# Performance work log

Measured on AMD Instinct MI355X. Metric: run time of the kernel, lower is better.

Reference implementation:

```python
import jax, jax.numpy as jnp
import numpy as np

# dims: StyleGAN2 modulated conv at 64x64, 512 channels
B, IC, OC, K, SD, H, W = 16, 512, 512, 3, 512, 64, 64
EPS = 1e-8


def setup_inputs() -> dict:
    key = jax.random.key(0)
    k1, k2, k3, k4 = jax.random.split(key, 4)
    return {
        "input": jax.random.normal(k1, (B, IC, H, W), dtype=jnp.float32),
        "style": jax.random.normal(k2, (B, SD), dtype=jnp.float32),
        # learned params
        "weight": jax.random.normal(k3, (1, OC, IC, K, K), dtype=jnp.float32),
        "mod_weight": jax.random.normal(k4, (IC, SD), dtype=jnp.float32),
        "mod_bias": jnp.ones((IC,), dtype=jnp.float32),  # bias_init=1
    }


def reference(input, style, weight, mod_weight, mod_bias):
    conv_scale = 1.0 / np.sqrt(IC * K * K)   # 1/sqrt(fan_in)
    mod_scale = 1.0 / np.sqrt(SD)            # EqualLinear scale, lr_mul=1

    # style modulation: EqualLinear(style_dim -> in_channel), no activation
    s = style @ (mod_weight * mod_scale).T + mod_bias          # [B, IC]

    # per-sample modulated weight [B, OC, IC, K, K]
    w = conv_scale * weight * s[:, None, :, None, None]
    # demodulation over (in_channel, kh, kw)
    demod = jax.lax.rsqrt(jnp.sum(w * w, axis=(2, 3, 4)) + EPS)  # [B, OC]
    w = w * demod[:, :, None, None, None]

    # grouped conv with groups=batch (same trick as torch F.conv2d groups=B)
    x = input.reshape(1, B * IC, H, W)
    wg = w.reshape(B * OC, IC, K, K)
    pad = K // 2
    out = jax.lax.conv_general_dilated(
        x, wg,
        window_strides=(1, 1),
        padding=[(pad, pad), (pad, pad)],
        dimension_numbers=("NCHW", "OIHW", "NCHW"),
        feature_group_count=B,
    )
    return out.reshape(B, OC, H, W)
```

## Files before the change

### kernel.cpp

```cpp
#include <hip/hip_runtime.h>
#include <hip/hip_bf16.h>

constexpr int BB = 16, IC = 512, OC = 512, HH = 64, WW = 64, HW = 64 * 64, SD = 512;
constexpr float MOD_SCALE = 0.04419417382415922f;
constexpr float CONV_SCALE = 0.014731391274719739f;
constexpr float CONV_SCALE2 = 2.170138888888889e-4f;

typedef float f32x4 __attribute__((ext_vector_type(4)));
typedef short bf16x8 __attribute__((ext_vector_type(8)));

#define VMWAIT(n) asm volatile("s_waitcnt vmcnt(" #n ")" ::: "memory")

__device__ __forceinline__ unsigned short f2bf(float x) {
  __hip_bfloat16 h = __float2bfloat16(x);
  return *(unsigned short*)&h;
}

__global__ void k_style(const float* __restrict__ style, const float* __restrict__ mw,
                        const float* __restrict__ mb, float* __restrict__ s) {
  __shared__ float st[SD];
  const int b = blockIdx.x;
  for (int i = threadIdx.x; i < SD; i += 256) st[i] = style[b * SD + i];
  __syncthreads();
  for (int ic = threadIdx.x; ic < IC; ic += 256) {
    const float4* wr = (const float4*)(mw + (size_t)ic * SD);
    float acc = 0.f;
    for (int d = 0; d < SD / 4; ++d) {
      float4 w4 = wr[d];
      float4 s4 = *(const float4*)&st[d * 4];
      acc += w4.x * s4.x + w4.y * s4.y + w4.z * s4.z + w4.w * s4.w;
    }
    s[b * IC + ic] = acc * MOD_SCALE + mb[ic];
  }
}

__global__ void k_pack(const float* __restrict__ w, unsigned short* __restrict__ wpack,
                       float* __restrict__ w2sum) {
  const int oc = blockIdx.x;
  const int ic0 = threadIdx.x * 2;
  const float* p = w + (size_t)oc * IC * 9 + (size_t)ic0 * 9;
  float v[18];
#pragma unroll
  for (int i = 0; i < 18; ++i) v[i] = p[i];
  float s0 = 0.f, s1 = 0.f;
#pragma unroll
  for (int t = 0; t < 9; ++t) { s0 += v[t] * v[t]; s1 += v[9 + t] * v[9 + t]; }
  *(float2*)&w2sum[oc * IC + ic0] = make_float2(s0, s1);
#pragma unroll
  for (int t = 0; t < 9; ++t) {
    unsigned int pk = (unsigned int)f2bf(v[t]) | ((unsigned int)f2bf(v[9 + t]) << 16);
    *(unsigned int*)&wpack[((size_t)t * OC + oc) * IC + ic0] = pk;
  }
}

__global__ void k_demod(const float* __restrict__ s, const float* __restrict__ w2sum,
                        float* __restrict__ fscale) {
  __shared__ float s2[IC];
  const int b = blockIdx.x;
  for (int i = threadIdx.x; i < IC; i += 256) { float v = s[b * IC + i]; s2[i] = v * v; }
  __syncthreads();
  for (int oc = threadIdx.x; oc < OC; oc += 256) {
    const float4* wr = (const float4*)(w2sum + (size_t)oc * IC);
    float acc = 0.f;
    for (int i4 = 0; i4 < IC / 4; ++i4) {
      float4 w4 = wr[i4];
      float4 q4 = *(const float4*)&s2[i4 * 4];
      acc += w4.x * q4.x + w4.y * q4.y + w4.z * q4.z + w4.w * q4.w;
    }
    fscale[b * OC + oc] = CONV_SCALE * rsqrtf(CONV_SCALE2 * acc + 1e-8f);
  }
}

#define LOADB(DST, TN)                                                         \
  do {                                                                         \
    const int dh_ = (TN) / 3 - 1, dw_ = (TN) % 3 - 1;                          \
    const int hb_ = wn + dh_ + 1;                                              \
    _Pragma("unroll") for (int j_ = 0; j_ < 4; ++j_) {                         \
      int r_ = hb_ * 66 + j_ * 16 + lrow + dw_ + 1;                            \
      DST[j_] = *(const bf16x8*)&Bsm[r_ * 32 + ((lk ^ ((r_ >> 1) & 3)) * 8)];  \
    }                                                                          \
  } while (0)

#define TAP_MFMA(USE, PRE, T)                                                  \
  do {                                                                         \
    __builtin_amdgcn_s_setprio(1);                                             \
    _Pragma("unroll") for (int j_ = 0; j_ < 4; ++j_)                           \
      acc[0][j_] = __builtin_amdgcn_mfma_f32_16x16x32_bf16(af[0], USE[j_],     \
                                                           acc[0][j_], 0, 0, 0); \
    if ((T) < 8) { LOADB(PRE, (T) + 1); }                                      \
    _Pragma("unroll") for (int i_ = 1; i_ < 4; ++i_)                           \
      _Pragma("unroll") for (int j_ = 0; j_ < 4; ++j_)                         \
        acc[i_][j_] = __builtin_amdgcn_mfma_f32_16x16x32_bf16(af[i_], USE[j_], \
                                                              acc[i_][j_], 0, 0, 0); \
    __builtin_amdgcn_s_setprio(0);                                             \
  } while (0)

__global__ __launch_bounds__(256, 3) void k_conv(
    const float* __restrict__ x, const unsigned short* __restrict__ wpack,
    const float* __restrict__ s, const float* __restrict__ fscale,
    float* __restrict__ out) {
  __shared__ __align__(128) unsigned short Asm[3][128 * 32];
  __shared__ __align__(128) unsigned short Bsm[264 * 32];

  const int bx = blockIdx.x;
  const int b = bx >> 7;
  const int mblk = (bx >> 5) & 3;
  const int nblk = bx & 31;

  const int tid = threadIdx.x;
  const int wave = tid >> 6, lane = tid & 63;
  const int wm = wave >> 1, wn = wave & 1;
  const int lrow = lane & 15, lk = lane >> 4;

  const int h0 = nblk * 2;
  const float* xb = x + (size_t)b * IC * HW;
  const float* sb = s + b * IC;

  f32x4 acc[4][4];
#pragma unroll
  for (int i = 0; i < 4; ++i)
#pragma unroll
    for (int j = 0; j < 4; ++j) acc[i][j] = f32x4{0.f, 0.f, 0.f, 0.f};

  {
    int q = tid >> 5;
    int hh = q >> 1, wz = (q & 1) ? 65 : 0;
    Bsm[(hh * 66 + wz) * 32 + (tid & 31)] = 0;
  }

  auto stageB = [&](int icb) {
    const int hh = wave;
    const int w = lane;
    const int h_abs = h0 - 1 + hh;
    const bool vh = (h_abs >= 0) && (h_abs < HH);
    const int h_safe = vh ? h_abs : 0;
    const int r = hh * 66 + w + 1;
    const int swz = (r >> 1) & 3;
    const float* src = xb + (size_t)(icb * 32) * HW + h_safe * WW + w;
#pragma unroll
    for (int c = 0; c < 4; ++c) {
      unsigned int pk[4];
#pragma unroll
      for (int jj = 0; jj < 4; ++jj) {
        int ic = c * 8 + jj * 2;
        float m0 = vh ? sb[icb * 32 + ic] : 0.f;
        float m1 = vh ? sb[icb * 32 + ic + 1] : 0.f;
        float v0 = src[(size_t)ic * HW] * m0;
        float v1 = src[(size_t)(ic + 1) * HW] * m1;
        pk[jj] = (unsigned int)f2bf(v0) | ((unsigned int)f2bf(v1) << 16);
      }
      int cd = c ^ swz;
      *(uint4*)&Bsm[r * 32 + cd * 8] = make_uint4(pk[0], pk[1], pk[2], pk[3]);
    }
  };

  auto issueA = [&](int tap, int icb, int nb) {
    const unsigned short* base =
        wpack + ((size_t)(tap * OC + mblk * 128)) * IC + icb * 32;
#pragma unroll
    for (int q = 0; q < 2; ++q) {
      int r = wave * 32 + q * 16 + (lane >> 2);
      int cs = (lane & 3) ^ ((r >> 1) & 3);
      const unsigned short* g = base + (size_t)r * IC + cs * 8;
      unsigned short* l = &Asm[nb][(wave * 32 + q * 16) * 32];
      __builtin_amdgcn_global_load_lds(
          (const __attribute__((address_space(1))) void*)g,
          (__attribute__((address_space(3))) void*)l, 16, 0, 0);
    }
  };

  stageB(0);
  issueA(0, 0, 0);
  issueA(1, 0, 1);
  __syncthreads();

  bf16x8 bcur[4], bnxt[4];

  for (int icb = 0; icb < 16; ++icb) {
#pragma unroll
    for (int t = 0; t < 9; ++t) {
      if (t == 8) {
        if (icb == 15) { VMWAIT(0); } else { VMWAIT(2); }
      } else {
        VMWAIT(2);
      }
      __builtin_amdgcn_s_barrier();
      __builtin_amdgcn_sched_barrier(0);

      if (t == 0) {
        if (icb > 0) {
          stageB(icb);
          asm volatile("s_waitcnt lgkmcnt(0)" ::: "memory");
          __builtin_amdgcn_s_barrier();
          __builtin_amdgcn_sched_barrier(0);
        }
        LOADB(bcur, 0);
      }

      if (t <= 6) {
        issueA(t + 2, icb, (t + 2) % 3);
      } else if (icb < 15) {
        issueA(t - 7, icb + 1, t - 7);
      }

      bf16x8 af[4];
#pragma unroll
      for (int i = 0; i < 4; ++i) {
        int r = wm * 64 + i * 16 + lrow;
        af[i] = *(const bf16x8*)&Asm[t % 3][r * 32 + ((lk ^ ((r >> 1) & 3)) * 8)];
      }

      if ((t & 1) == 0) {
        TAP_MFMA(bcur, bnxt, t);
      } else {
        TAP_MFMA(bnxt, bcur, t);
      }
      __builtin_amdgcn_sched_barrier(0);
    }
  }

  const float* fsb = fscale + b * OC;
#pragma unroll
  for (int i = 0; i < 4; ++i) {
#pragma unroll
    for (int rr = 0; rr < 4; ++rr) {
      const int oc = mblk * 128 + wm * 64 + i * 16 + lk * 4 + rr;
      const float sc = fsb[oc];
      float* orow = out + ((size_t)(b * OC + oc)) * HW + nblk * 128 + wn * 64 + lrow;
#pragma unroll
      for (int j = 0; j < 4; ++j) orow[j * 16] = acc[i][j][rr] * sc;
    }
  }
}

extern "C" void kernel_launch(void* const* d_in, const int* in_sizes, int n_in,
                              void* d_out, int out_size, void* d_ws, size_t ws_size,
                              hipStream_t stream) {
  const float* input = (const float*)d_in[0];
  const float* style = (const float*)d_in[1];
  const float* weight = (const float*)d_in[2];
  const float* mod_weight = (const float*)d_in[3];
  const float* mod_bias = (const float*)d_in[4];
  float* out = (float*)d_out;

  char* ws = (char*)d_ws;
  constexpr size_t WPACK_B = (size_t)9 * OC * IC * 2;
  constexpr size_t W2SUM_B = (size_t)OC * IC * 4;
  constexpr size_t S_B = (size_t)BB * IC * 4;
  unsigned short* wpack = (unsigned short*)ws;
  float* w2sum = (float*)(ws + WPACK_B);
  float* s = (float*)(ws + WPACK_B + W2SUM_B);
  float* fscale = (float*)(ws + WPACK_B + W2SUM_B + S_B);

  k_style<<<BB, 256, 0, stream>>>(style, mod_weight, mod_bias, s);
  k_pack<<<OC, 256, 0, stream>>>(weight, wpack, w2sum);
  k_demod<<<BB, 256, 0, stream>>>(s, w2sum, fscale);
  k_conv<<<2048, 256, 0, stream>>>(input, wpack, s, fscale, out);
}
```

Before: 460.9 us.

## Load weight fragments directly from global into registers, drop LDS A buffer

Replaces the triple-buffered LDS staging of the packed weights (global_load_lds) with direct per-lane global loads of A fragments into registers, prefetched one tap ahead. B fragments are now read from LDS right before each tap's MFMAs. The block index is also remapped so that consecutive launched blocks spread across batches and tiles, changing L2 locality. Weight loads are no longer shared across waves, and their latency is exposed with only one tap of prefetch. Removing the per-tap vmcnt waits may also leave a global load unwaited in places.

```diff
diff --git a/kernel.cpp b/kernel.cpp
--- a/kernel.cpp
+++ b/kernel.cpp
@@ -8,8 +8,6 @@
 
 typedef float f32x4 __attribute__((ext_vector_type(4)));
 typedef short bf16x8 __attribute__((ext_vector_type(8)));
-
-#define VMWAIT(n) asm volatile("s_waitcnt vmcnt(" #n ")" ::: "memory")
 
 __device__ __forceinline__ unsigned short f2bf(float x) {
   __hip_bfloat16 h = __float2bfloat16(x);
@@ -71,6 +69,14 @@
   }
 }
 
+#define LOADA(DST, TN, ICB)                                                    \
+  do {                                                                         \
+    _Pragma("unroll") for (int i_ = 0; i_ < 4; ++i_) {                         \
+      DST[i_] = *(const bf16x8*)(wpA + ((size_t)(TN)*OC + i_ * 16) * IC +      \
+                                 (size_t)(ICB) * 32);                          \
+    }                                                                          \
+  } while (0)
+
 #define LOADB(DST, TN)                                                         \
   do {                                                                         \
     const int dh_ = (TN) / 3 - 1, dw_ = (TN) % 3 - 1;                          \
@@ -81,16 +87,15 @@
     }                                                                          \
   } while (0)
 
-#define TAP_MFMA(USE, PRE, T)                                                  \
+#define TAP(USE, PRE, T, ICB)                                                  \
   do {                                                                         \
+    if ((T) < 8) { LOADA(PRE, (T) + 1, ICB); }                                 \
+    bf16x8 bfr[4];                                                             \
+    LOADB(bfr, (T));                                                           \
     __builtin_amdgcn_s_setprio(1);                                             \
-    _Pragma("unroll") for (int j_ = 0; j_ < 4; ++j_)                           \
-      acc[0][j_] = __builtin_amdgcn_mfma_f32_16x16x32_bf16(af[0], USE[j_],     \
-                                                           acc[0][j_], 0, 0, 0); \
-    if ((T) < 8) { LOADB(PRE, (T) + 1); }                                      \
-    _Pragma("unroll") for (int i_ = 1; i_ < 4; ++i_)                           \
+    _Pragma("unroll") for (int i_ = 0; i_ < 4; ++i_)                           \
       _Pragma("unroll") for (int j_ = 0; j_ < 4; ++j_)                         \
-        acc[i_][j_] = __builtin_amdgcn_mfma_f32_16x16x32_bf16(af[i_], USE[j_], \
+        acc[i_][j_] = __builtin_amdgcn_mfma_f32_16x16x32_bf16(USE[i_], bfr[j_],\
                                                               acc[i_][j_], 0, 0, 0); \
     __builtin_amdgcn_s_setprio(0);                                             \
   } while (0)
@@ -99,10 +104,9 @@
     const float* __restrict__ x, const unsigned short* __restrict__ wpack,
     const float* __restrict__ s, const float* __restrict__ fscale,
     float* __restrict__ out) {
-  __shared__ __align__(128) unsigned short Asm[3][128 * 32];
   __shared__ __align__(128) unsigned short Bsm[264 * 32];
 
-  const int bx = blockIdx.x;
+  const int bx = ((blockIdx.x & 7) << 8) | (blockIdx.x >> 3);
   const int b = bx >> 7;
   const int mblk = (bx >> 5) & 3;
   const int nblk = bx & 31;
@@ -115,6 +119,9 @@
   const int h0 = nblk * 2;
   const float* xb = x + (size_t)b * IC * HW;
   const float* sb = s + b * IC;
+
+  const unsigned short* wpA =
+      wpack + ((size_t)(mblk * 128 + wm * 64 + lrow)) * IC + lk * 8;
 
   f32x4 acc[4][4];
 #pragma unroll
@@ -154,68 +161,35 @@
     }
   };
 
-  auto issueA = [&](int tap, int icb, int nb) {
-    const unsigned short* base =
-        wpack + ((size_t)(tap * OC + mblk * 128)) * IC + icb * 32;
-#pragma unroll
-    for (int q = 0; q < 2; ++q) {
-      int r = wave * 32 + q * 16 + (lane >> 2);
-      int cs = (lane & 3) ^ ((r >> 1) & 3);
-      const unsigned short* g = base + (size_t)r * IC + cs * 8;
-      unsigned short* l = &Asm[nb][(wave * 32 + q * 16) * 32];
-      __builtin_amdgcn_global_load_lds(
-          (const __attribute__((address_space(1))) void*)g,
-          (__attribute__((address_space(3))) void*)l, 16, 0, 0);
-    }
-  };
-
   stageB(0);
-  issueA(0, 0, 0);
-  issueA(1, 0, 1);
-  __syncthreads();
-
-  bf16x8 bcur[4], bnxt[4];
+  asm volatile("s_waitcnt lgkmcnt(0)" ::: "memory");
+  __builtin_amdgcn_s_barrier();
+
+  bf16x8 afA[4], afB[4];
 
   for (int icb = 0; icb < 16; ++icb) {
+    LOADA(afA, 0, icb);
 #pragma unroll
     for (int t = 0; t < 9; ++t) {
-      if (t == 8) {
-        if (icb == 15) { VMWAIT(0); } else { VMWAIT(2); }
+      if (t > 0) {
+        __builtin_amdgcn_s_barrier();
+        __builtin_amdgcn_sched_barrier(0);
+      }
+      if ((t & 1) == 0) {
+        TAP(afA, afB, t, icb);
       } else {
-        VMWAIT(2);
+        TAP(afB, afA, t, icb);
       }
+      __builtin_amdgcn_sched_barrier(0);
+    }
+
+    if (icb < 15) {
       __builtin_amdgcn_s_barrier();
       __builtin_amdgcn_sched_barrier(0);
-
-      if (t == 0) {
-        if (icb > 0) {
-          stageB(icb);
-          asm volatile("s_waitcnt lgkmcnt(0)" ::: "memory");
-          __builtin_amdgcn_s_barrier();
-          __builtin_amdgcn_sched_barrier(0);
-        }
-        LOADB(bcur, 0);
-      }
-
-      if (t <= 6) {
-        issueA(t + 2, icb, (t + 2) % 3);
-      } else if (icb < 15) {
-        issueA(t - 7, icb + 1, t - 7);
-      }
-
-      bf16x8 af[4];
-#pragma unroll
-      for (int i = 0; i < 4; ++i) {
-        int r = wm * 64 + i * 16 + lrow;
-        af[i] = *(const bf16x8*)&Asm[t % 3][r * 32 + ((lk ^ ((r >> 1) & 3)) * 8)];
-      }
-
-      if ((t & 1) == 0) {
-        TAP_MFMA(bcur, bnxt, t);
-      } else {
-        TAP_MFMA(bnxt, bcur, t);
-      }
+      stageB(icb + 1);
+      asm volatile("s_waitcnt lgkmcnt(0)" ::: "memory");
       __builtin_amdgcn_sched_barrier(0);
+      __builtin_amdgcn_s_barrier();
     }
   }
 
```

Result: slower. 663.2 us (+43.9%).
